# Optimization experiments

Hardware: AMD Instinct MI355X
Metric: run time of the kernel (lower is better)

Reference implementation:

```python
import jax, jax.numpy as jnp
import numpy as np

B, NQ, NK = 4, 1024, 1536
DQ = DK = DV = 1024
DI = 4096
H = 16
EPS = 1e-5

def _ln(x, g, b):
    mu = jnp.mean(x, axis=-1, keepdims=True)
    var = jnp.mean((x - mu) ** 2, axis=-1, keepdims=True)
    return (x - mu) * jax.lax.rsqrt(var + EPS) * g + b

def setup_inputs() -> dict:
    key = jax.random.key(0)
    ks = jax.random.split(key, 20)
    s = 0.02
    inp = {
        "Q": jax.random.normal(ks[0], (B, NQ, DQ), jnp.float32),
        "K": jax.random.normal(ks[1], (B, NK, DK), jnp.float32),
        "knn_masks": jax.random.normal(ks[2], (B * H, NQ, 1024), jnp.float32),
        "mask_pos": 1024,
        "Wq": jax.random.normal(ks[3], (DQ, DV), jnp.float32) * s,
        "bq": jnp.zeros((DV,), jnp.float32),
        "Wk": jax.random.normal(ks[4], (DK, DV), jnp.float32) * s,
        "bk": jnp.zeros((DV,), jnp.float32),
        "Wv": jax.random.normal(ks[5], (DK, DV), jnp.float32) * s,
        "bv": jnp.zeros((DV,), jnp.float32),
        "Wo0": jax.random.normal(ks[6], (DV, DV), jnp.float32) * s,
        "bo0": jnp.zeros((DV,), jnp.float32),
        "Wo": jax.random.normal(ks[7], (DV, DI), jnp.float32) * s,
        "bo": jnp.zeros((DI,), jnp.float32),
        "Wo2": jax.random.normal(ks[8], (DI, DV), jnp.float32) * s,
        "bo2": jnp.zeros((DV,), jnp.float32),
        "g0": jnp.ones((DV,), jnp.float32),
        "beta0": jnp.zeros((DV,), jnp.float32),
        "g1": jnp.ones((DV,), jnp.float32),
        "beta1": jnp.zeros((DV,), jnp.float32),
    }
    return inp

def reference(Q, K, knn_masks, mask_pos, Wq, bq, Wk, bk, Wv, bv,
              Wo0, bo0, Wo, bo, Wo2, bo2, g0, beta0, g1, beta1):
    dh = DV // H
    q = Q @ Wq + bq                      # [B,NQ,DV]
    k = K @ Wk + bk                      # [B,NK,DV]
    v = K @ Wv + bv
    # torch cat(split(.,dh,2),0) -> head-major [H,B,N,dh]
    qh = q.reshape(B, NQ, H, dh).transpose(2, 0, 1, 3)
    kh = k[:, :mask_pos].reshape(B, mask_pos, H, dh).transpose(2, 0, 1, 3)
    vh = v[:, :mask_pos].reshape(B, mask_pos, H, dh).transpose(2, 0, 1, 3)
    logits = jnp.einsum("hbqd,hbkd->hbqk", qh, kh) / jnp.sqrt(jnp.float32(DV))
    logits = logits + knn_masks.reshape(H, B, NQ, mask_pos)
    attn = jax.nn.softmax(logits, axis=-1)
    o = jnp.einsum("hbqk,hbkd->hbqd", attn, vh)   # [H,B,NQ,dh]
    o = o.transpose(1, 2, 0, 3).reshape(B, NQ, DV)  # concat heads
    o = o @ Wo0 + bo0
    O = q + o
    O = _ln(O, g0, beta0)
    ff = jax.nn.relu(O @ Wo + bo) @ Wo2 + bo2
    O = O + ff
    O = _ln(O, g1, beta1)
    return O
```

## Files before the change

kernel.cpp:

```cpp
#include <hip/hip_runtime.h>
#include <hip/hip_bf16.h>

typedef unsigned short u16;
typedef __attribute__((ext_vector_type(4))) short bf16x4;
typedef __attribute__((ext_vector_type(8))) short bf16x8;
typedef __attribute__((ext_vector_type(4))) float f32x4;

static __device__ __forceinline__ u16 f2b(float f){
  union { float f; unsigned u; } v; v.f = f;
  unsigned r = v.u + 0x7fffu + ((v.u >> 16) & 1u);
  return (u16)(r >> 16);
}
static __device__ __forceinline__ float b2f(u16 h){
  union { unsigned u; float f; } v; v.u = ((unsigned)h) << 16; return v.f;
}
static __device__ __forceinline__ void gld_lds16(const void* g, void* l){
  __builtin_amdgcn_global_load_lds((const __attribute__((address_space(1))) void*)g,
                                   (__attribute__((address_space(3))) void*)l, 16, 0, 0);
}

__global__ __launch_bounds__(256) void prep(const float* __restrict__ Q,
                                            const float* __restrict__ K,
                                            u16* __restrict__ Qb, u16* __restrict__ Kb,
                                            const float* __restrict__ Wq, u16* __restrict__ Wq_t,
                                            const float* __restrict__ Wk, u16* __restrict__ Wk_t,
                                            const float* __restrict__ Wv, u16* __restrict__ Wv_t,
                                            const float* __restrict__ Wo0, u16* __restrict__ Wo0_t,
                                            const float* __restrict__ Wo, u16* __restrict__ Wo_t,
                                            const float* __restrict__ Wo2, u16* __restrict__ Wo2_t){
  __shared__ float tile[64][65];
  const int id = blockIdx.x, t = threadIdx.x;
  if (id < 8192){
    const float* src; u16* dst;
    if (id < 4096){
      src = Q + (size_t)id * 1024; dst = Qb + (size_t)id * 1024;
    } else {
      int r = id - 4096;
      size_t ir = (size_t)r + (size_t)(r >> 10) * 512;
      src = K + ir * 1024; dst = Kb + (size_t)r * 1024;
    }
    const float4 v = *(const float4*)(src + t * 4);
    bf16x4 o;
    o[0] = (short)f2b(v.x); o[1] = (short)f2b(v.y);
    o[2] = (short)f2b(v.z); o[3] = (short)f2b(v.w);
    *(bf16x4*)(dst + t * 4) = o;
    return;
  }
  int wid = id - 8192;
  const float* in; u16* out; int Kd, N, bx, by;
  if (wid < 1024){
    int sel = wid >> 8, local = wid & 255;
    bx = local & 15; by = local >> 4; Kd = 1024; N = 1024;
    in  = (sel == 0) ? Wq   : (sel == 1) ? Wk   : (sel == 2) ? Wv   : Wo0;
    out = (sel == 0) ? Wq_t : (sel == 1) ? Wk_t : (sel == 2) ? Wv_t : Wo0_t;
  } else if (wid < 2048){
    int local = wid - 1024; bx = local & 63; by = local >> 6; Kd = 1024; N = 4096;
    in = Wo; out = Wo_t;
  } else {
    int local = wid - 2048; bx = local & 15; by = local >> 4; Kd = 4096; N = 1024;
    in = Wo2; out = Wo2_t;
  }
  const int k0 = by * 64, n0 = bx * 64;
  const int tr = t >> 4, tc = t & 15;
#pragma unroll
  for (int i = 0; i < 4; i++){
    int r = tr + i * 16;
    float4 v = *(const float4*)(in + (size_t)(k0 + r) * N + n0 + tc * 4);
    tile[r][tc*4+0] = v.x; tile[r][tc*4+1] = v.y; tile[r][tc*4+2] = v.z; tile[r][tc*4+3] = v.w;
  }
  __syncthreads();
#pragma unroll
  for (int i = 0; i < 4; i++){
    int nr = tr + i * 16;
    bf16x4 pk;
#pragma unroll
    for (int j = 0; j < 4; j++) pk[j] = (short)f2b(tile[tc*4+j][nr]);
    *(bf16x4*)(out + (size_t)(n0 + nr) * Kd + k0 + tc * 4) = pk;
  }
}

static __device__ __forceinline__ void loop8p(const u16* __restrict__ A,
                                              const u16* __restrict__ Bt,
                                              int lda, int ldb, int kbeg, int NT,
                                              int m0, int n0,
                                              u16 (*sA)[2][8192], u16 (*sB)[2][8192],
                                              f32x4 acc[8][4]){
  const int t = threadIdx.x, w = t >> 6, l = t & 63;
  const int wr = w >> 2, wc = w & 3;
  const int c = l & 15, g = l >> 4;
  const int sr = t >> 3, scb = (t & 7) << 4;

  auto stA = [&](int d, int h, int T){
#pragma unroll
    for (int i = 0; i < 2; i++){
      int row = i * 64 + sr;
      int Lb  = scb ^ ((row & 7) << 4);
      gld_lds16(A + (size_t)(m0 + h * 128 + row) * lda + kbeg + T * 64 + (Lb >> 1),
                (char*)&sA[d][h][0] + i * 8192 + t * 16);
    }
  };
  auto stB = [&](int d, int h, int T){
#pragma unroll
    for (int i = 0; i < 2; i++){
      int row = i * 64 + sr;
      int Lb  = scb ^ ((row & 7) << 4);
      gld_lds16(Bt + (size_t)(n0 + h * 128 + row) * ldb + kbeg + T * 64 + (Lb >> 1),
                (char*)&sB[d][h][0] + i * 8192 + t * 16);
    }
  };

  stB(0, 0, 0); stB(0, 1, 0); stA(0, 0, 0); stA(0, 1, 0);
  stB(1, 0, 1); stB(1, 1, 1);

  bf16x8 bfr[4][2];
  for (int T = 0; T < NT; ++T){
    const int d = T & 1;
    const char* pa = (const char*)&sA[d][wr][0];
    const char* pb = (const char*)&sB[d][wc >> 1][0];
#pragma unroll
    for (int q = 0; q < 4; ++q){
      if (q == 0){
        if (T + 1 < NT) asm volatile("s_waitcnt vmcnt(4)" ::: "memory");
        else            asm volatile("s_waitcnt vmcnt(0)" ::: "memory");
        asm volatile("" ::: "memory");
        __builtin_amdgcn_s_barrier();
        asm volatile("" ::: "memory");
#pragma unroll
        for (int nf = 0; nf < 4; ++nf){
          int lr = (wc & 1) * 64 + nf * 16 + c;
#pragma unroll
          for (int ks = 0; ks < 2; ++ks)
            bfr[nf][ks] = *(const bf16x8*)(pb + lr * 128 + ((ks * 64 + g * 16) ^ ((lr & 7) << 4)));
        }
      }
      bf16x8 af[2][2];
#pragma unroll
      for (int mi = 0; mi < 2; ++mi){
        int lr = (q * 2 + mi) * 16 + c;
#pragma unroll
        for (int ks = 0; ks < 2; ++ks)
          af[mi][ks] = *(const bf16x8*)(pa + lr * 128 + ((ks * 64 + g * 16) ^ ((lr & 7) << 4)));
      }
      if      (q == 0){ if (T + 1 < NT) stA(d ^ 1, 0, T + 1); }
      else if (q == 1){ if (T + 1 < NT) stA(d ^ 1, 1, T + 1); }
      else if (q == 2){ if (T + 2 < NT) stB(d, 0, T + 2); }
      else            { if (T + 2 < NT) stB(d, 1, T + 2); }
      __builtin_amdgcn_s_setprio(1);
#pragma unroll
      for (int mi = 0; mi < 2; ++mi)
#pragma unroll
        for (int nf = 0; nf < 4; ++nf)
#pragma unroll
          for (int ks = 0; ks < 2; ++ks)
            acc[q * 2 + mi][nf] =
              __builtin_amdgcn_mfma_f32_16x16x32_bf16(af[mi][ks], bfr[nf][ks], acc[q * 2 + mi][nf], 0, 0, 0);
      __builtin_amdgcn_s_setprio(0);
      asm volatile("" ::: "memory");
      __builtin_amdgcn_s_barrier();
      asm volatile("" ::: "memory");
    }
  }
}

template<int EPI>
__global__ __launch_bounds__(512, 2) void gemm8p(const u16* __restrict__ A,
                                                 const u16* __restrict__ Bt,
                                                 const float* __restrict__ bias,
                                                 void* __restrict__ outp,
                                                 int lda, int ldb, int ldout,
                                                 int ksz, int NT){
  __shared__ u16 sA[2][2][8192];
  __shared__ u16 sB[2][2][8192];
  const int t = threadIdx.x, w = t >> 6, l = t & 63;
  const int wr = w >> 2, wc = w & 3;
  const int c = l & 15, g = l >> 4;

  int m0, n0, zidx;
  if (EPI == 0){
    int lid = blockIdx.x + (blockIdx.y << 4);
    int xcd = lid & 7, slot = lid >> 3;
    int bx = ((xcd & 1) << 3) + (slot & 7);
    int by = ((xcd >> 1) << 2) + (slot >> 3);
    m0 = by * 256; n0 = bx * 256; zidx = 0;
  } else {
    int lid = blockIdx.x + (blockIdx.y << 2) + (blockIdx.z << 6);
    int xcd = lid & 7, slot = lid >> 3;
    int bx = slot & 3, rest = slot >> 2;
    int by = (xcd << 1) + (rest & 1);
    zidx = rest >> 1;
    m0 = by * 256; n0 = bx * 256;
  }

  f32x4 acc[8][4];
#pragma unroll
  for (int i = 0; i < 8; i++)
#pragma unroll
    for (int j = 0; j < 4; j++) acc[i][j] = (f32x4){0.f, 0.f, 0.f, 0.f};

  loop8p(A, Bt, lda, ldb, zidx * ksz, NT, m0, n0, sA, sB, acc);

  if (EPI == 0){
    u16* out = (u16*)outp;
#pragma unroll
    for (int nf = 0; nf < 4; ++nf){
      int n = n0 + wc * 64 + nf * 16 + c;
      float bv = bias[n];
#pragma unroll
      for (int mf = 0; mf < 8; ++mf){
        int row0 = m0 + wr * 128 + mf * 16 + 4 * g;
#pragma unroll
        for (int r = 0; r < 4; ++r)
          out[(size_t)(row0 + r) * ldout + n] = f2b(fmaxf(acc[mf][nf][r] + bv, 0.f));
      }
    }
  } else {
    u16* po = (u16*)outp + (size_t)zidx * (4096ull * 1024ull);
#pragma unroll
    for (int nf = 0; nf < 4; ++nf){
      int n = n0 + wc * 64 + nf * 16 + c;
#pragma unroll
      for (int mf = 0; mf < 8; ++mf){
        int row0 = m0 + wr * 128 + mf * 16 + 4 * g;
#pragma unroll
        for (int r = 0; r < 4; ++r)
          po[(size_t)(row0 + r) * 1024 + n] = f2b(acc[mf][nf][r]);
      }
    }
  }
}

__global__ __launch_bounds__(512, 2) void gemm8p_qkv(const u16* __restrict__ Qb,
                                                     const u16* __restrict__ Kb,
                                                     const u16* __restrict__ Wq_t,
                                                     const u16* __restrict__ Wk_t,
                                                     const u16* __restrict__ Wv_t,
                                                     const float* __restrict__ bq,
                                                     const float* __restrict__ bk,
                                                     const float* __restrict__ bv,
                                                     u16* __restrict__ qb,
                                                     u16* __restrict__ kbf,
                                                     u16* __restrict__ vtb){
  __shared__ u16 sA[2][2][8192];
  __shared__ u16 sB[2][2][8192];
  int lid = blockIdx.x + blockIdx.y * 12;
  int xcd = lid & 7, slot = lid >> 3;
  int bx = (xcd & 3) * 3 + slot % 3;
  int by = ((xcd >> 2) << 3) + slot / 3;
  const int sel = bx >> 2;
  const u16* A    = sel ? Kb : Qb;
  const u16* Bt   = (sel == 0) ? Wq_t : (sel == 1) ? Wk_t : Wv_t;
  const float* bi = (sel == 0) ? bq   : (sel == 1) ? bk   : bv;
  const int t = threadIdx.x, w = t >> 6, l = t & 63;
  const int wr = w >> 2, wc = w & 3;
  const int c = l & 15, g = l >> 4;
  const int m0 = by * 256, n0 = (bx & 3) * 256;

  f32x4 acc[8][4];
#pragma unroll
  for (int i = 0; i < 8; i++)
#pragma unroll
    for (int j = 0; j < 4; j++) acc[i][j] = (f32x4){0.f, 0.f, 0.f, 0.f};

  loop8p(A, Bt, 1024, 1024, 0, 16, m0, n0, sA, sB, acc);

  if (sel == 2){
    u16* sl = (w < 4) ? (&sA[0][0][0] + w * 8192) : (&sB[0][0][0] + (w - 4) * 8192);
#pragma unroll
    for (int nf = 0; nf < 4; ++nf){
      int n = n0 + wc * 64 + nf * 16 + c;
      float bv_ = bi[n];
#pragma unroll
      for (int mf = 0; mf < 8; ++mf){
        bf16x4 pk;
#pragma unroll
        for (int r = 0; r < 4; ++r) pk[r] = (short)f2b(acc[mf][nf][r] + bv_);
        *(bf16x4*)(sl + (nf * 16 + c) * 128 + mf * 16 + 4 * g) = pk;
      }
    }
    asm volatile("s_waitcnt lgkmcnt(0)" ::: "memory");
    __builtin_amdgcn_sched_barrier(0);
    const int mg = m0 + wr * 128;
    const int bb = mg >> 10, kb0 = mg & 1023;
    u16* vbase = vtb + ((size_t)bb << 20) + kb0;
#pragma unroll
    for (int j = 0; j < 16; ++j){
      int nl  = (l >> 4) + j * 4;
      int kl  = (l & 15) * 8;
      bf16x8 v = *(const bf16x8*)(sl + nl * 128 + kl);
      *(bf16x8*)(vbase + (size_t)(n0 + wc * 64 + nl) * 1024 + kl) = v;
    }
  } else {
    u16* out = sel ? kbf : qb;
#pragma unroll
    for (int nf = 0; nf < 4; ++nf){
      int n = n0 + wc * 64 + nf * 16 + c;
      float bv_ = bi[n];
#pragma unroll
      for (int mf = 0; mf < 8; ++mf){
        int row0 = m0 + wr * 128 + mf * 16 + 4 * g;
#pragma unroll
        for (int r = 0; r < 4; ++r)
          out[(size_t)(row0 + r) * 1024 + n] = f2b(acc[mf][nf][r] + bv_);
      }
    }
  }
}

template<int NP, int F32OUT>
__global__ __launch_bounds__(256) void comb_ln(const u16* __restrict__ pp,
                                               const float* __restrict__ bias,
                                               const u16* __restrict__ res,
                                               const float* __restrict__ gw,
                                               const float* __restrict__ bw,
                                               void* __restrict__ outp){
  const int t = threadIdx.x, w = t >> 6;
  const int row = blockIdx.x * 2 + (t >> 7);
  const int u = t & 127;
  const size_t i8 = (size_t)row * 1024 + u * 8;
  bf16x8 rv = *(const bf16x8*)(res + i8);
  float4 b0 = *(const float4*)(bias + u * 8);
  float4 b1 = *(const float4*)(bias + u * 8 + 4);
  float xs[8] = {b0.x, b0.y, b0.z, b0.w, b1.x, b1.y, b1.z, b1.w};
#pragma unroll
  for (int j = 0; j < 8; j++) xs[j] += b2f((u16)rv[j]);
#pragma unroll
  for (int z = 0; z < NP; z++){
    bf16x8 p = *(const bf16x8*)(pp + (size_t)z * (4096ull * 1024ull) + i8);
#pragma unroll
    for (int j = 0; j < 8; j++) xs[j] += b2f((u16)p[j]);
  }
  float s = 0.f, sq = 0.f;
#pragma unroll
  for (int j = 0; j < 8; j++){ s += xs[j]; sq += xs[j] * xs[j]; }
#pragma unroll
  for (int o = 32; o; o >>= 1){ s += __shfl_xor(s, o); sq += __shfl_xor(sq, o); }
  __shared__ float rs[4], rq[4];
  if ((t & 63) == 0){ rs[w] = s; rq[w] = sq; }
  __syncthreads();
  const int wb = (t >> 7) * 2;
  s  = rs[wb] + rs[wb + 1];
  sq = rq[wb] + rq[wb + 1];
  const float mu   = s * (1.f / 1024.f);
  const float var  = sq * (1.f / 1024.f) - mu * mu;
  const float rstd = rsqrtf(var + 1e-5f);
  float4 g0 = *(const float4*)(gw + u * 8);
  float4 g1 = *(const float4*)(gw + u * 8 + 4);
  float4 w0 = *(const float4*)(bw + u * 8);
  float4 w1 = *(const float4*)(bw + u * 8 + 4);
  float gv[8] = {g0.x, g0.y, g0.z, g0.w, g1.x, g1.y, g1.z, g1.w};
  float wv[8] = {w0.x, w0.y, w0.z, w0.w, w1.x, w1.y, w1.z, w1.w};
  if (F32OUT){
    float4 o0, o1;
    o0.x = (xs[0]-mu)*rstd*gv[0] + wv[0]; o0.y = (xs[1]-mu)*rstd*gv[1] + wv[1];
    o0.z = (xs[2]-mu)*rstd*gv[2] + wv[2]; o0.w = (xs[3]-mu)*rstd*gv[3] + wv[3];
    o1.x = (xs[4]-mu)*rstd*gv[4] + wv[4]; o1.y = (xs[5]-mu)*rstd*gv[5] + wv[5];
    o1.z = (xs[6]-mu)*rstd*gv[6] + wv[6]; o1.w = (xs[7]-mu)*rstd*gv[7] + wv[7];
    *(float4*)((float*)outp + i8)     = o0;
    *(float4*)((float*)outp + i8 + 4) = o1;
  } else {
    bf16x8 o;
#pragma unroll
    for (int j = 0; j < 8; j++) o[j] = (short)f2b((xs[j]-mu)*rstd*gv[j] + wv[j]);
    *(bf16x8*)((u16*)outp + i8) = o;
  }
}

#define ATTN_STEP(IT, CUR, MC) do{                                              \
  if ((IT) < 15) asm volatile("s_waitcnt vmcnt(4)" ::: "memory");               \
  else           asm volatile("s_waitcnt vmcnt(0)" ::: "memory");               \
  __builtin_amdgcn_s_barrier();                                                 \
  asm volatile("" ::: "memory");                                                \
  if ((IT) < 15) stage((CUR) ^ 1, ((IT) + 1) * 64);                             \
  asm volatile("" ::: "memory");                                                \
  const char* kt = (const char*)sK[(CUR)];                                      \
  f32x4 st[4];                                                                  \
  _Pragma("unroll")                                                             \
  for (int nf = 0; nf < 4; nf++){                                               \
    const char* kr = kt + (nf * 16 + c) * 128;                                  \
    bf16x8 ak0 = *(const bf16x8*)(kr + ((g * 16) ^ sw));                        \
    bf16x8 ak1 = *(const bf16x8*)(kr + ((64 + g * 16) ^ sw));                   \
    f32x4 z = (f32x4){0.f, 0.f, 0.f, 0.f};                                      \
    z = __builtin_amdgcn_mfma_f32_16x16x32_bf16(ak0, bq0, z, 0, 0, 0);          \
    z = __builtin_amdgcn_mfma_f32_16x16x32_bf16(ak1, bq1, z, 0, 0, 0);          \
    st[nf] = z;                                                                 \
  }                                                                             \
  float rsum = 0.f;                                                             \
  bf16x4 pb[4];                                                                 \
  _Pragma("unroll")                                                             \
  for (int nf = 0; nf < 4; nf++)                                                \
    _Pragma("unroll")                                                           \
    for (int r = 0; r < 4; r++){                                                \
      float p = __expf(fmaf(st[nf][r], 0.03125f, MC[nf][r]) - 8.f);             \
      rsum += p;                                                                \
      pb[nf][r] = (short)f2b(p);                                                \
    }                                                                           \
  if ((IT) < 14){                                                               \
    _Pragma("unroll")                                                           \
    for (int nf = 0; nf < 4; nf++)                                              \
      MC[nf] = *(const f32x4*)(mbase + ((IT) + 2) * 64 + nf * 16 + g * 4);      \
  }                                                                             \
  rsum += __shfl_xor(rsum, 16); rsum += __shfl_xor(rsum, 32);                   \
  lsum += rsum;                                                                 \
  const char* vtc = (const char*)sV[(CUR)];                                     \
  __builtin_amdgcn_s_setprio(1);                                                \
  _Pragma("unroll")                                                             \
  for (int f = 0; f < 4; f++){                                                  \
    const char* vr = vtc + (f * 16 + c) * 128;                                  \
    _Pragma("unroll")                                                           \
    for (int nf = 0; nf < 4; nf++){                                             \
      bf16x4 av = *(const bf16x4*)(vr + ((nf * 32 + g * 8) ^ sw));              \
      acc[f] = __builtin_amdgcn_mfma_f32_16x16x16bf16_1k(av, pb[nf], acc[f], 0, 0, 0); \
    }                                                                           \
  }                                                                             \
  __builtin_amdgcn_s_setprio(0);                                                \
}while(0)

__global__ __launch_bounds__(256, 4) void attn_k(const u16* __restrict__ qb,
                                                 const u16* __restrict__ kb,
                                                 const u16* __restrict__ vt,
                                                 const float* __restrict__ mask,
                                                 u16* __restrict__ ob){
  __shared__ u16 sK[2][4096];
  __shared__ u16 sV[2][4096];

  const int t = threadIdx.x, w = t >> 6, l = t & 63;
  const int c = l & 15, g = l >> 4;
  const int lid  = blockIdx.x + (blockIdx.y << 4) + (blockIdx.z << 8);
  const int xcd  = lid & 7, slot = lid >> 3;
  const int grp  = xcd + ((slot >> 4) << 3);
  const int q0   = (slot & 15) * 64;
  const int h    = grp & 15, b = grp >> 4;
  const int qrow = q0 + w * 16 + c;
  const size_t qoff = ((size_t)(b * 1024 + qrow)) * 1024 + h * 64;
  const bf16x8 bq0 = *(const bf16x8*)(qb + qoff + g * 8);
  const bf16x8 bq1 = *(const bf16x8*)(qb + qoff + 32 + g * 8);
  const u16* kbase = kb + ((size_t)b * 1024) * 1024 + h * 64;
  const u16* vbase = vt + ((size_t)b << 20) + (size_t)(h * 64) * 1024;
  const float* mbase = mask + ((size_t)(h * 4 + b) * 1024 + qrow) * 1024;

  const int lr3 = l >> 3, lc3 = l & 7;
  const int ch0 = w * 2;

  auto stage = [&](int buf, int kv){
#pragma unroll
    for (int i = 0; i < 2; i++){
      int ch  = ch0 + i;
      int row = ch * 8 + lr3;
      int L   = (lc3 * 16) ^ ((row & 7) << 4);
      gld_lds16(kbase + (size_t)(kv + row) * 1024 + (L >> 1), &sK[buf][ch * 512]);
      gld_lds16(vbase + (size_t)row * 1024 + kv + (L >> 1),   &sV[buf][ch * 512]);
    }
  };

  float lsum = 0.f;
  f32x4 acc[4];
#pragma unroll
  for (int f = 0; f < 4; f++) acc[f] = (f32x4){0.f, 0.f, 0.f, 0.f};

  stage(0, 0);
  asm volatile("" ::: "memory");
  f32x4 mA[4], mB[4];
#pragma unroll
  for (int nf = 0; nf < 4; nf++) mA[nf] = *(const f32x4*)(mbase + nf * 16 + g * 4);
  asm volatile("" ::: "memory");
#pragma unroll
  for (int nf = 0; nf < 4; nf++) mB[nf] = *(const f32x4*)(mbase + 64 + nf * 16 + g * 4);

  const int sw = (c & 7) << 4;
  for (int ii = 0; ii < 8; ++ii){
    ATTN_STEP(2 * ii,     0, mA);
    ATTN_STEP(2 * ii + 1, 1, mB);
  }

  const float inv = 1.f / lsum;
  u16* sO = &sK[0][0];
#pragma unroll
  for (int f = 0; f < 4; f++){
    bf16x4 pk;
#pragma unroll
    for (int r = 0; r < 4; r++) pk[r] = (short)f2b(acc[f][r] * inv);
    *(bf16x4*)(sO + (w * 16 + c) * 64 + f * 16 + 4 * g) = pk;
  }
  asm volatile("s_waitcnt lgkmcnt(0)" ::: "memory");
  __builtin_amdgcn_sched_barrier(0);
  {
    int rl  = w * 16 + (l >> 2);
    int d0  = (l & 3) * 16;
    bf16x8 v0 = *(const bf16x8*)(sO + rl * 64 + d0);
    bf16x8 v1 = *(const bf16x8*)(sO + rl * 64 + d0 + 8);
    u16* dst = ob + ((size_t)(b * 1024 + q0 + rl)) * 1024 + h * 64 + d0;
    *(bf16x8*)(dst)     = v0;
    *(bf16x8*)(dst + 8) = v1;
  }
}

extern "C" void kernel_launch(void* const* d_in, const int* in_sizes, int n_in,
                              void* d_out, int out_size, void* d_ws, size_t ws_size,
                              hipStream_t stream){
  const float* Q    = (const float*)d_in[0];
  const float* K    = (const float*)d_in[1];
  const float* mask = (const float*)d_in[2];
  const float* Wq   = (const float*)d_in[4];  const float* bq  = (const float*)d_in[5];
  const float* Wk   = (const float*)d_in[6];  const float* bk  = (const float*)d_in[7];
  const float* Wv   = (const float*)d_in[8];  const float* bv  = (const float*)d_in[9];
  const float* Wo0  = (const float*)d_in[10]; const float* bo0 = (const float*)d_in[11];
  const float* Wo   = (const float*)d_in[12]; const float* bo  = (const float*)d_in[13];
  const float* Wo2  = (const float*)d_in[14]; const float* bo2 = (const float*)d_in[15];
  const float* g0   = (const float*)d_in[16]; const float* be0 = (const float*)d_in[17];
  const float* g1   = (const float*)d_in[18]; const float* be1 = (const float*)d_in[19];

  uint8_t* W = (uint8_t*)d_ws;
  const size_t MB = 1024ull * 1024ull;
  u16* Wq_t  = (u16*)(W + 0);
  u16* Wk_t  = (u16*)(W + 2  * MB);
  u16* Wv_t  = (u16*)(W + 4  * MB);
  u16* Wo0_t = (u16*)(W + 6  * MB);
  u16* Wo_t  = (u16*)(W + 8  * MB);
  u16* Wo2_t = (u16*)(W + 16 * MB);
  u16* Qb    = (u16*)(W + 24 * MB);
  u16* Kb    = (u16*)(W + 32 * MB);
  u16* qb    = (u16*)(W + 40 * MB);
  u16* kbf   = (u16*)(W + 48 * MB);
  u16* vtb   = (u16*)(W + 56 * MB);
  u16* ob    = (u16*)(W + 24 * MB);
  u16* x1b   = (u16*)(W + 64 * MB);
  u16* hb    = (u16*)(W + 32 * MB);
  u16* ppb   = (u16*)(W + 72 * MB);

  prep<<<11264, 256, 0, stream>>>(Q, K, Qb, Kb, Wq, Wq_t, Wk, Wk_t, Wv, Wv_t,
                                  Wo0, Wo0_t, Wo, Wo_t, Wo2, Wo2_t);

  gemm8p_qkv<<<dim3(12, 16), 512, 0, stream>>>(Qb, Kb, Wq_t, Wk_t, Wv_t,
                                               bq, bk, bv, qb, kbf, vtb);

  attn_k<<<dim3(16, 16, 4), 256, 0, stream>>>(qb, kbf, vtb, mask, ob);

  gemm8p<1><<<dim3(4, 16, 4), 512, 0, stream>>>(ob, Wo0_t, nullptr, ppb, 1024, 1024, 1024, 256, 4);
  comb_ln<4, 0><<<2048, 256, 0, stream>>>(ppb, bo0, qb, g0, be0, x1b);

  gemm8p<0><<<dim3(16, 16), 512, 0, stream>>>(x1b, Wo_t, bo, hb, 1024, 1024, 4096, 0, 16);
  gemm8p<1><<<dim3(4, 16, 4), 512, 0, stream>>>(hb, Wo2_t, nullptr, ppb, 4096, 4096, 1024, 1024, 16);
  comb_ln<4, 1><<<2048, 256, 0, stream>>>(ppb, bo2, x1b, g1, be1, d_out);
}
```

Baseline: 291.5 us.

## Fold output-weight transposes into attention kernel and widen attention blocks to 128 rows

```diff
diff --git a/kernel.cpp b/kernel.cpp
--- a/kernel.cpp
+++ b/kernel.cpp
@@ -24,10 +24,7 @@
                                             u16* __restrict__ Qb, u16* __restrict__ Kb,
                                             const float* __restrict__ Wq, u16* __restrict__ Wq_t,
                                             const float* __restrict__ Wk, u16* __restrict__ Wk_t,
-                                            const float* __restrict__ Wv, u16* __restrict__ Wv_t,
-                                            const float* __restrict__ Wo0, u16* __restrict__ Wo0_t,
-                                            const float* __restrict__ Wo, u16* __restrict__ Wo_t,
-                                            const float* __restrict__ Wo2, u16* __restrict__ Wo2_t){
+                                            const float* __restrict__ Wv, u16* __restrict__ Wv_t){
   __shared__ float tile[64][65];
   const int id = blockIdx.x, t = threadIdx.x;
   if (id < 8192){
@@ -47,25 +44,16 @@
     return;
   }
   int wid = id - 8192;
-  const float* in; u16* out; int Kd, N, bx, by;
-  if (wid < 1024){
-    int sel = wid >> 8, local = wid & 255;
-    bx = local & 15; by = local >> 4; Kd = 1024; N = 1024;
-    in  = (sel == 0) ? Wq   : (sel == 1) ? Wk   : (sel == 2) ? Wv   : Wo0;
-    out = (sel == 0) ? Wq_t : (sel == 1) ? Wk_t : (sel == 2) ? Wv_t : Wo0_t;
-  } else if (wid < 2048){
-    int local = wid - 1024; bx = local & 63; by = local >> 6; Kd = 1024; N = 4096;
-    in = Wo; out = Wo_t;
-  } else {
-    int local = wid - 2048; bx = local & 15; by = local >> 4; Kd = 4096; N = 1024;
-    in = Wo2; out = Wo2_t;
-  }
+  int sel = wid >> 8, local = wid & 255;
+  int bx = local & 15, by = local >> 4;
+  const float* in  = (sel == 0) ? Wq   : (sel == 1) ? Wk   : Wv;
+  u16*         out = (sel == 0) ? Wq_t : (sel == 1) ? Wk_t : Wv_t;
   const int k0 = by * 64, n0 = bx * 64;
   const int tr = t >> 4, tc = t & 15;
 #pragma unroll
   for (int i = 0; i < 4; i++){
     int r = tr + i * 16;
-    float4 v = *(const float4*)(in + (size_t)(k0 + r) * N + n0 + tc * 4);
+    float4 v = *(const float4*)(in + (size_t)(k0 + r) * 1024 + n0 + tc * 4);
     tile[r][tc*4+0] = v.x; tile[r][tc*4+1] = v.y; tile[r][tc*4+2] = v.z; tile[r][tc*4+3] = v.w;
   }
   __syncthreads();
@@ -75,7 +63,7 @@
     bf16x4 pk;
 #pragma unroll
     for (int j = 0; j < 4; j++) pk[j] = (short)f2b(tile[tc*4+j][nr]);
-    *(bf16x4*)(out + (size_t)(n0 + nr) * Kd + k0 + tc * 4) = pk;
+    *(bf16x4*)(out + (size_t)(n0 + nr) * 1024 + k0 + tc * 4) = pk;
   }
 }
 
@@ -415,21 +403,57 @@
   __builtin_amdgcn_s_setprio(0);                                                \
 }while(0)
 
-__global__ __launch_bounds__(256, 4) void attn_k(const u16* __restrict__ qb,
+__global__ __launch_bounds__(512, 4) void attn_k(const u16* __restrict__ qb,
                                                  const u16* __restrict__ kb,
                                                  const u16* __restrict__ vt,
                                                  const float* __restrict__ mask,
-                                                 u16* __restrict__ ob){
+                                                 u16* __restrict__ ob,
+                                                 const float* __restrict__ Wo0, u16* __restrict__ Wo0_t,
+                                                 const float* __restrict__ Wo,  u16* __restrict__ Wo_t,
+                                                 const float* __restrict__ Wo2, u16* __restrict__ Wo2_t){
   __shared__ u16 sK[2][4096];
   __shared__ u16 sV[2][4096];
 
-  const int t = threadIdx.x, w = t >> 6, l = t & 63;
+  const int id = blockIdx.x, t = threadIdx.x;
+
+  if (id < 1152){
+    const int half = t >> 8, tt = t & 255;
+    const int tileid = id * 2 + half;
+    const float* in; u16* out; int Kd, N, bx, by;
+    if (tileid < 256){
+      bx = tileid & 15; by = tileid >> 4; Kd = 1024; N = 1024; in = Wo0; out = Wo0_t;
+    } else if (tileid < 1280){
+      int lo = tileid - 256; bx = lo & 63; by = lo >> 6; Kd = 1024; N = 4096; in = Wo; out = Wo_t;
+    } else {
+      int lo = tileid - 1280; bx = lo & 15; by = lo >> 4; Kd = 4096; N = 1024; in = Wo2; out = Wo2_t;
+    }
+    u16* tl = half ? &sV[0][0] : &sK[0][0];
+    const int k0 = by * 64, n0 = bx * 64;
+    const int tr = tt >> 4, tc = tt & 15;
+#pragma unroll
+    for (int i = 0; i < 4; i++){
+      int r = tr + i * 16;
+      float4 v = *(const float4*)(in + (size_t)(k0 + r) * N + n0 + tc * 4);
+      tl[r * 65 + tc * 4 + 0] = f2b(v.x); tl[r * 65 + tc * 4 + 1] = f2b(v.y);
+      tl[r * 65 + tc * 4 + 2] = f2b(v.z); tl[r * 65 + tc * 4 + 3] = f2b(v.w);
+    }
+    __syncthreads();
+#pragma unroll
+    for (int i = 0; i < 4; i++){
+      int nr = tr + i * 16;
+      bf16x4 pk;
+#pragma unroll
+      for (int j = 0; j < 4; j++) pk[j] = (short)tl[(tc * 4 + j) * 65 + nr];
+      *(bf16x4*)(out + (size_t)(n0 + nr) * Kd + k0 + tc * 4) = pk;
+    }
+    return;
+  }
+
+  const int aid = id - 1152;
+  const int w = t >> 6, l = t & 63;
   const int c = l & 15, g = l >> 4;
-  const int lid  = blockIdx.x + (blockIdx.y << 4) + (blockIdx.z << 8);
-  const int xcd  = lid & 7, slot = lid >> 3;
-  const int grp  = xcd + ((slot >> 4) << 3);
-  const int q0   = (slot & 15) * 64;
-  const int h    = grp & 15, b = grp >> 4;
+  const int q0 = (aid & 7) * 128;
+  const int h  = (aid >> 3) & 15, b = aid >> 7;
   const int qrow = q0 + w * 16 + c;
   const size_t qoff = ((size_t)(b * 1024 + qrow)) * 1024 + h * 64;
   const bf16x8 bq0 = *(const bf16x8*)(qb + qoff + g * 8);
@@ -438,18 +462,12 @@
   const u16* vbase = vt + ((size_t)b << 20) + (size_t)(h * 64) * 1024;
   const float* mbase = mask + ((size_t)(h * 4 + b) * 1024 + qrow) * 1024;
 
-  const int lr3 = l >> 3, lc3 = l & 7;
-  const int ch0 = w * 2;
+  const int srow = t >> 3, slc = t & 7;
 
   auto stage = [&](int buf, int kv){
-#pragma unroll
-    for (int i = 0; i < 2; i++){
-      int ch  = ch0 + i;
-      int row = ch * 8 + lr3;
-      int L   = (lc3 * 16) ^ ((row & 7) << 4);
-      gld_lds16(kbase + (size_t)(kv + row) * 1024 + (L >> 1), &sK[buf][ch * 512]);
-      gld_lds16(vbase + (size_t)row * 1024 + kv + (L >> 1),   &sV[buf][ch * 512]);
-    }
+    int L = (slc * 16) ^ ((srow & 7) << 4);
+    gld_lds16(kbase + (size_t)(kv + srow) * 1024 + (L >> 1), &sK[buf][t * 8]);
+    gld_lds16(vbase + (size_t)srow * 1024 + kv + (L >> 1),   &sV[buf][t * 8]);
   };
 
   float lsum = 0.f;
@@ -472,6 +490,7 @@
     ATTN_STEP(2 * ii + 1, 1, mB);
   }
 
+  __syncthreads();
   const float inv = 1.f / lsum;
   u16* sO = &sK[0][0];
 #pragma unroll
@@ -527,13 +546,13 @@
   u16* hb    = (u16*)(W + 32 * MB);
   u16* ppb   = (u16*)(W + 72 * MB);
 
-  prep<<<11264, 256, 0, stream>>>(Q, K, Qb, Kb, Wq, Wq_t, Wk, Wk_t, Wv, Wv_t,
-                                  Wo0, Wo0_t, Wo, Wo_t, Wo2, Wo2_t);
+  prep<<<8960, 256, 0, stream>>>(Q, K, Qb, Kb, Wq, Wq_t, Wk, Wk_t, Wv, Wv_t);
 
   gemm8p_qkv<<<dim3(12, 16), 512, 0, stream>>>(Qb, Kb, Wq_t, Wk_t, Wv_t,
                                                bq, bk, bv, qb, kbf, vtb);
 
-  attn_k<<<dim3(16, 16, 4), 256, 0, stream>>>(qb, kbf, vtb, mask, ob);
+  attn_k<<<1664, 512, 0, stream>>>(qb, kbf, vtb, mask, ob,
+                                   Wo0, Wo0_t, Wo, Wo_t, Wo2, Wo2_t);
 
   gemm8p<1><<<dim3(4, 16, 4), 512, 0, stream>>>(ob, Wo0_t, nullptr, ppb, 1024, 1024, 1024, 256, 4);
   comb_ln<4, 0><<<2048, 256, 0, stream>>>(ppb, bo0, qb, g0, be0, x1b);
```

Measured after the change: 290.1 us. Within noise of the previous version (-0.5%).
